# Optimization experiments

Hardware: AMD Instinct MI355X
Metric: run time of the kernel (lower is better)

The kernel has to match this reference:

```python
import jax, jax.numpy as jnp
import numpy as np

Q, D, DIM, VOCAB = 4096, 32768, 128, 32000


def setup_inputs() -> dict:
    key = jax.random.key(0)
    k1, k2, k3, k4, k5, k6 = jax.random.split(key, 6)
    return {
        "query_embeddings": jax.random.normal(k1, (Q, DIM), dtype=jnp.float32),
        "doc_embeddings": jax.random.normal(k2, (D, DIM), dtype=jnp.float32),
        "query_token_ids": jax.random.randint(k3, (Q,), 0, VOCAB, dtype=jnp.int32),
        "doc_token_ids": jax.random.randint(k4, (D,), 0, VOCAB, dtype=jnp.int32),
        "query_weight_table": jax.random.uniform(k5, (VOCAB,), dtype=jnp.float32),
        "doc_weight_table": jax.random.uniform(k6, (VOCAB,), dtype=jnp.float32),
    }


def reference(query_embeddings, doc_embeddings, query_token_ids, doc_token_ids,
              query_weight_table, doc_weight_table):
    # token-level MaxSim: [Q, D] similarity, max over doc tokens
    sim = jnp.einsum('qd,kd->qk', query_embeddings, doc_embeddings)  # [Q, D]
    max_sim = jnp.max(sim, axis=1)          # [Q]
    max_idx = jnp.argmax(sim, axis=1)       # [Q]

    # token_weighter: learned scalar weight per token id
    query_weights = query_weight_table[query_token_ids]             # [Q]
    best_doc_ids = doc_token_ids[max_idx]                           # [Q] device-side gather
    doc_weights = doc_weight_table[best_doc_ids]                    # [Q]

    combined = query_weights * doc_weights                          # [Q]
    # 'linear' normalization with zero-sum fallback to uniform weights
    wsum = jnp.sum(combined)
    safe = jnp.where(wsum > 0, wsum, jnp.float32(1.0))
    uniform = jnp.full_like(combined, 1.0 / combined.shape[0])
    normalized = jnp.where(wsum > 0, combined / safe, uniform)

    return jnp.sum(max_sim * normalized)
```

## Files before the change

### kernel.cpp

```cpp
#include <hip/hip_runtime.h>
#include <hip/hip_bf16.h>
#include <stdint.h>

#define Q_N   4096
#define D_N   32768
#define DIM   128
#define VOCAB 32000

#define NCHUNK 32
#define CHUNK  (D_N / NCHUNK)
#define QTILE  256
#define NQT    (Q_N / QTILE)
#define DSUB   128
#define NSUB   (CHUNK / DSUB)
#define NSLOT  (NCHUNK * 2)

typedef short  short8 __attribute__((ext_vector_type(8)));
typedef float  f32x4  __attribute__((ext_vector_type(4)));

#define WS_QBF  0u
#define WS_DBF  0x100000u
#define WS_PMI  0x900000u
#define WS_SUMS 0xB00000u

__device__ inline ushort f2bf(float f) {
  uint32_t u = __float_as_uint(f);
  u += 0x7FFFu + ((u >> 16) & 1u);
  return (ushort)(u >> 16);
}

__global__ void convert_kernel(const float* __restrict__ qe, const float* __restrict__ de,
                               ushort* __restrict__ qb, ushort* __restrict__ db,
                               float* __restrict__ sums) {
  int i = blockIdx.x * 256 + threadIdx.x;
  if (i < 4) sums[i] = 0.0f;
  const int NQ4 = Q_N * DIM / 4;
  float4 v;
  ushort* dst;
  if (i < NQ4) {
    v = ((const float4*)qe)[i];
    dst = qb + (size_t)i * 4;
  } else {
    int j = i - NQ4;
    v = ((const float4*)de)[j];
    dst = db + (size_t)j * 4;
  }
  ushort4 o;
  o.x = f2bf(v.x); o.y = f2bf(v.y); o.z = f2bf(v.z); o.w = f2bf(v.w);
  *(ushort4*)dst = o;
}

__global__ __launch_bounds__(512, 4)
void maxsim_kernel(const ushort* __restrict__ dbf, const ushort* __restrict__ qbf,
                   float2* __restrict__ pmi) {
  __shared__ ushort lds[2][DSUB * DIM];

  const int tid  = threadIdx.x;
  const int lane = tid & 63;
  const int wid  = tid >> 6;
  const int wm   = wid >> 2;
  const int wn   = wid & 3;

  const int bid  = blockIdx.x;
  const int xcd  = bid & 7;
  const int slot = bid >> 3;
  const int c    = xcd + 8 * (slot >> 4);
  const int qt   = slot & 15;
  const int qblock = qt * QTILE;
  const int chunk0 = c * CHUNK;

  short8 bfr[4][4];
  #pragma unroll
  for (int nf = 0; nf < 4; ++nf) {
    int qrow = qblock + wn * 64 + nf * 16 + (lane & 15);
    const ushort* p = qbf + (size_t)qrow * DIM + ((lane >> 4) * 8);
    #pragma unroll
    for (int kk = 0; kk < 4; ++kk)
      bfr[nf][kk] = *(const short8*)(p + kk * 32);
  }

  float rmax[4]; int ridx[4];
  #pragma unroll
  for (int nf = 0; nf < 4; ++nf) { rmax[nf] = -3.0e38f; ridx[nf] = 0; }

  const char* gdoc = (const char*)(dbf + (size_t)chunk0 * DIM);

  int swzoff[4];
  #pragma unroll
  for (int it = 0; it < 4; ++it) {
    int o = wid * 4096 + it * 1024 + lane * 16;
    swzoff[it] = o ^ (((o >> 8) & 7) << 4);
  }

  auto stage = [&](int b, int st) {
    const char* gt = gdoc + st * (DSUB * DIM * 2);
    char* lb = (char*)&lds[b][0] + wid * 4096;
    #pragma unroll
    for (int it = 0; it < 4; ++it) {
      __builtin_amdgcn_global_load_lds(
          (const __attribute__((address_space(1))) uint32_t*)(gt + swzoff[it]),
          (__attribute__((address_space(3))) uint32_t*)(lb + it * 1024),
          16, 0, 0);
    }
  };

  stage(0, 0);
  __syncthreads();

  #pragma unroll 1
  for (int st = 0; st < NSUB; ++st) {
    const int b = st & 1;
    if (st + 1 < NSUB) stage(b ^ 1, st + 1);

    const char* lb = (const char*)&lds[b][0];
    #pragma unroll
    for (int mf = 0; mf < 4; ++mf) {
      short8 afr[4];
      int arow = wm * 64 + mf * 16 + (lane & 15);
      #pragma unroll
      for (int kk = 0; kk < 4; ++kk) {
        int abyte = (arow * 256 + kk * 64 + ((lane >> 4) * 16)) ^ ((arow & 7) << 4);
        afr[kk] = *(const short8*)(lb + abyte);
      }
      f32x4 acc[4];
      #pragma unroll
      for (int nf = 0; nf < 4; ++nf) acc[nf] = (f32x4){0.f, 0.f, 0.f, 0.f};
      #pragma unroll
      for (int kk = 0; kk < 4; ++kk)
        #pragma unroll
        for (int nf = 0; nf < 4; ++nf)
          acc[nf] = __builtin_amdgcn_mfma_f32_16x16x32_bf16(afr[kk], bfr[nf][kk], acc[nf], 0, 0, 0);
      const int code0 = st * 128 + wm * 64 + mf * 16;
      #pragma unroll
      for (int nf = 0; nf < 4; ++nf)
        #pragma unroll
        for (int r = 0; r < 4; ++r) {
          float v = acc[nf][r];
          bool gtv = v > rmax[nf];
          rmax[nf] = gtv ? v : rmax[nf];
          ridx[nf] = gtv ? (code0 + r) : ridx[nf];
        }
    }
    __syncthreads();
  }

  const int pslot = c * 2 + wm;
  #pragma unroll
  for (int nf = 0; nf < 4; ++nf) {
    float m = rmax[nf];
    int gi = chunk0 + ridx[nf] + ((lane >> 4) << 2);
    #pragma unroll
    for (int s = 16; s <= 32; s <<= 1) {
      float om = __shfl_xor(m, s);
      int   oi = __shfl_xor(gi, s);
      if (om > m || (om == m && oi < gi)) { m = om; gi = oi; }
    }
    if (lane < 16) {
      int q = qblock + wn * 64 + nf * 16 + lane;
      pmi[pslot * Q_N + q] = make_float2(m, __int_as_float(gi));
    }
  }
}

__global__ void reduce_kernel(const float2* __restrict__ pmi,
                              const int* __restrict__ qtok, const int* __restrict__ dtok,
                              const float* __restrict__ qwt, const float* __restrict__ dwt,
                              float* __restrict__ sums) {
  int q = blockIdx.x * 256 + threadIdx.x;
  float m = -3.0e38f; int best = 0;
  #pragma unroll 8
  for (int s = 0; s < NSLOT; ++s) {
    float2 p = pmi[s * Q_N + q];
    int i = __float_as_int(p.y);
    if (p.x > m || (p.x == m && i < best)) { m = p.x; best = i; }
  }
  float cmb = qwt[qtok[q]] * dwt[dtok[best]];
  float s0 = cmb, s1 = m * cmb, s2 = m;
  #pragma unroll
  for (int sh = 32; sh >= 1; sh >>= 1) {
    s0 += __shfl_down(s0, sh);
    s1 += __shfl_down(s1, sh);
    s2 += __shfl_down(s2, sh);
  }
  __shared__ float red[3][4];
  int lane = threadIdx.x & 63, w = threadIdx.x >> 6;
  if (lane == 0) { red[0][w] = s0; red[1][w] = s1; red[2][w] = s2; }
  __syncthreads();
  if (threadIdx.x == 0) {
    atomicAdd(&sums[0], red[0][0] + red[0][1] + red[0][2] + red[0][3]);
    atomicAdd(&sums[1], red[1][0] + red[1][1] + red[1][2] + red[1][3]);
    atomicAdd(&sums[2], red[2][0] + red[2][1] + red[2][2] + red[2][3]);
  }
}

__global__ void finalize_kernel(const float* __restrict__ sums, float* __restrict__ out) {
  float s0 = sums[0], s1 = sums[1], s2 = sums[2];
  out[0] = (s0 > 0.0f) ? (s1 / s0) : (s2 / (float)Q_N);
}

extern "C" void kernel_launch(void* const* d_in, const int* in_sizes, int n_in,
                              void* d_out, int out_size, void* d_ws, size_t ws_size,
                              hipStream_t stream) {
  const float* qe   = (const float*)d_in[0];
  const float* de   = (const float*)d_in[1];
  const int*   qtok = (const int*)d_in[2];
  const int*   dtok = (const int*)d_in[3];
  const float* qwt  = (const float*)d_in[4];
  const float* dwt  = (const float*)d_in[5];
  float* out = (float*)d_out;

  char* ws = (char*)d_ws;
  ushort* qbf  = (ushort*)(ws + WS_QBF);
  ushort* dbf  = (ushort*)(ws + WS_DBF);
  float2* pmi  = (float2*)(ws + WS_PMI);
  float*  sums = (float*)(ws + WS_SUMS);

  const int NQ4 = Q_N * DIM / 4, ND4 = D_N * DIM / 4;
  convert_kernel<<<(NQ4 + ND4) / 256, 256, 0, stream>>>(qe, de, qbf, dbf, sums);

  maxsim_kernel<<<NQT * NCHUNK, 512, 0, stream>>>(dbf, qbf, pmi);

  reduce_kernel<<<Q_N / 256, 256, 0, stream>>>(pmi, qtok, dtok, qwt, dwt, sums);
  finalize_kernel<<<1, 1, 0, stream>>>(sums, out);
}
```

Measured before the change: 139.0 us.

## Drop LDS staging in maxsim; load doc fragments directly from global

Removes the double-buffered LDS staging of document tiles and the per-step barrier. Each wave now reads its MFMA A-fragments straight from global memory. The block shrinks to 4 waves with a 128-query tile, giving twice as many blocks. This trades LDS traffic and sync overhead for more global/L2 reads, since doc rows are no longer shared across the waves that differ in wn, and the loads are uncoalesced 16-byte strided accesses.

Measured after the change: 167.8 us. 1.21x slower.

```diff
diff --git a/kernel.cpp b/kernel.cpp
--- a/kernel.cpp
+++ b/kernel.cpp
@@ -9,7 +9,7 @@
 
 #define NCHUNK 32
 #define CHUNK  (D_N / NCHUNK)
-#define QTILE  256
+#define QTILE  128
 #define NQT    (Q_N / QTILE)
 #define DSUB   128
 #define NSUB   (CHUNK / DSUB)
@@ -50,22 +50,20 @@
   *(ushort4*)dst = o;
 }
 
-__global__ __launch_bounds__(512, 4)
+__global__ __launch_bounds__(256, 4)
 void maxsim_kernel(const ushort* __restrict__ dbf, const ushort* __restrict__ qbf,
                    float2* __restrict__ pmi) {
-  __shared__ ushort lds[2][DSUB * DIM];
-
   const int tid  = threadIdx.x;
   const int lane = tid & 63;
   const int wid  = tid >> 6;
-  const int wm   = wid >> 2;
-  const int wn   = wid & 3;
+  const int wm   = wid >> 1;
+  const int wn   = wid & 1;
 
   const int bid  = blockIdx.x;
   const int xcd  = bid & 7;
   const int slot = bid >> 3;
-  const int c    = xcd + 8 * (slot >> 4);
-  const int qt   = slot & 15;
+  const int c    = xcd + 8 * (slot >> 5);
+  const int qt   = slot & 31;
   const int qblock = qt * QTILE;
   const int chunk0 = c * CHUNK;
 
@@ -83,45 +81,19 @@
   #pragma unroll
   for (int nf = 0; nf < 4; ++nf) { rmax[nf] = -3.0e38f; ridx[nf] = 0; }
 
-  const char* gdoc = (const char*)(dbf + (size_t)chunk0 * DIM);
-
-  int swzoff[4];
-  #pragma unroll
-  for (int it = 0; it < 4; ++it) {
-    int o = wid * 4096 + it * 1024 + lane * 16;
-    swzoff[it] = o ^ (((o >> 8) & 7) << 4);
-  }
-
-  auto stage = [&](int b, int st) {
-    const char* gt = gdoc + st * (DSUB * DIM * 2);
-    char* lb = (char*)&lds[b][0] + wid * 4096;
-    #pragma unroll
-    for (int it = 0; it < 4; ++it) {
-      __builtin_amdgcn_global_load_lds(
-          (const __attribute__((address_space(1))) uint32_t*)(gt + swzoff[it]),
-          (__attribute__((address_space(3))) uint32_t*)(lb + it * 1024),
-          16, 0, 0);
-    }
-  };
-
-  stage(0, 0);
-  __syncthreads();
+  const ushort* abase = dbf + (size_t)(chunk0 + wm * 64 + (lane & 15)) * DIM
+                            + ((lane >> 4) * 8);
 
   #pragma unroll 1
-  for (int st = 0; st < NSUB; ++st) {
-    const int b = st & 1;
-    if (st + 1 < NSUB) stage(b ^ 1, st + 1);
-
-    const char* lb = (const char*)&lds[b][0];
+  for (int dsu = 0; dsu < NSUB; ++dsu) {
+    const ushort* dsb = abase + dsu * (DSUB * DIM);
     #pragma unroll
     for (int mf = 0; mf < 4; ++mf) {
+      const ushort* mrow = dsb + mf * (16 * DIM);
       short8 afr[4];
-      int arow = wm * 64 + mf * 16 + (lane & 15);
       #pragma unroll
-      for (int kk = 0; kk < 4; ++kk) {
-        int abyte = (arow * 256 + kk * 64 + ((lane >> 4) * 16)) ^ ((arow & 7) << 4);
-        afr[kk] = *(const short8*)(lb + abyte);
-      }
+      for (int kk = 0; kk < 4; ++kk)
+        afr[kk] = *(const short8*)(mrow + kk * 32);
       f32x4 acc[4];
       #pragma unroll
       for (int nf = 0; nf < 4; ++nf) acc[nf] = (f32x4){0.f, 0.f, 0.f, 0.f};
@@ -130,7 +102,7 @@
         #pragma unroll
         for (int nf = 0; nf < 4; ++nf)
           acc[nf] = __builtin_amdgcn_mfma_f32_16x16x32_bf16(afr[kk], bfr[nf][kk], acc[nf], 0, 0, 0);
-      const int code0 = st * 128 + wm * 64 + mf * 16;
+      const int code0 = dsu * 128 + wm * 64 + mf * 16;
       #pragma unroll
       for (int nf = 0; nf < 4; ++nf)
         #pragma unroll
@@ -141,7 +113,6 @@
           ridx[nf] = gtv ? (code0 + r) : ridx[nf];
         }
     }
-    __syncthreads();
   }
 
   const int pslot = c * 2 + wm;
@@ -218,7 +189,7 @@
   const int NQ4 = Q_N * DIM / 4, ND4 = D_N * DIM / 4;
   convert_kernel<<<(NQ4 + ND4) / 256, 256, 0, stream>>>(qe, de, qbf, dbf, sums);
 
-  maxsim_kernel<<<NQT * NCHUNK, 512, 0, stream>>>(dbf, qbf, pmi);
+  maxsim_kernel<<<NQT * NCHUNK, 256, 0, stream>>>(dbf, qbf, pmi);
 
   reduce_kernel<<<Q_N / 256, 256, 0, stream>>>(pmi, qtok, dtok, qwt, dwt, sums);
   finalize_kernel<<<1, 1, 0, stream>>>(sums, out);
```
